# Performance work log

Measured on AMD Instinct MI355X. Metric: run time of the kernel, lower is better.

The kernel has to match this reference:

```python
import jax, jax.numpy as jnp
import numpy as np

H = 2048       # hidden_size
I = 5504       # intermediate_size
E = 8          # num_experts
TOPK = 2       # num_experts_per_tok


def setup_inputs() -> dict:
    key = jax.random.key(0)
    ks = jax.random.split(key, 5)
    s = 0.02
    x = jax.random.normal(ks[0], (2, 2048, H), dtype=jnp.float32)
    router_w = jax.random.normal(ks[1], (E, H), dtype=jnp.float32) * s   # Linear weight [out,in]
    Wg = jax.random.normal(ks[2], (E, I, H), dtype=jnp.float32) * s      # gate_proj per expert
    Wu = jax.random.normal(ks[3], (E, I, H), dtype=jnp.float32) * s      # up_proj per expert
    Wd = jax.random.normal(ks[4], (E, H, I), dtype=jnp.float32) * s      # down_proj per expert
    return {"x": x, "router_w": router_w, "Wg": Wg, "Wu": Wu, "Wd": Wd}


def reference(x, router_w, Wg, Wu, Wd):
    B, S, Hh = x.shape
    xf = x.reshape(-1, Hh)                                  # [T, H]
    logits = xf @ router_w.T                                # [T, E]
    top_vals, top_idx = jax.lax.top_k(logits, TOPK)         # [T, K]
    top_w = jax.nn.softmax(top_vals, axis=-1)               # softmax over selected logits only
    # combine weight per (token, expert): zero if expert not selected
    combine = jnp.sum(jax.nn.one_hot(top_idx, E, dtype=xf.dtype) * top_w[..., None], axis=1)  # [T, E]

    out = jnp.zeros_like(xf)
    for e in range(E):  # fixed small expert loop (unrolled under jit)
        h = jax.nn.silu(xf @ Wg[e].T) * (xf @ Wu[e].T)      # [T, I]
        y = h @ Wd[e].T                                     # [T, H]
        out = out + combine[:, e:e + 1] * y
    return out.reshape(B, S, Hh)
```

## Files before the change

kernel.cpp:

```cpp
#include <hip/hip_runtime.h>
#include <cstdint>
#include <cstddef>

#define HDIM 2048
#define IDIM 5504
#define NEXP 8
#define NTOK 4096
#define NROWS (2 * NTOK)

#define NCT1 86
#define NRT1 10
#define NWG1 (NCT1 * NRT1 * NEXP)
#define NK1  (HDIM / 32)
#define NCT2 8
#define NRT2 10
#define NWG2 (NCT2 * NRT2 * NEXP)
#define NK2  (IDIM / 32)
#define WDCH (NEXP * HDIM * IDIM / 8)

typedef _Float16 half8 __attribute__((ext_vector_type(8)));
typedef _Float16 half4v __attribute__((ext_vector_type(4)));
typedef float floatx4 __attribute__((ext_vector_type(4)));

#define GLOAD16(g, l)                                                         \
  __builtin_amdgcn_global_load_lds(                                           \
      (const __attribute__((address_space(1))) void*)(g),                     \
      (__attribute__((address_space(3))) void*)(l), 16, 0, 0)

#define XH_OFF   0
#define HB_OFF   (XH_OFF + (size_t)NTOK * HDIM * 2)
#define BTOK_OFF (HB_OFF + (size_t)NROWS * IDIM * 2)
#define BW_OFF   (BTOK_OFF + 32768)
#define TOKP_OFF (BW_OFF + 32768)
#define TOKW_OFF (TOKP_OFF + 16384)
#define T2R_OFF  (TOKW_OFF + 32768)
#define META_OFF (T2R_OFF + 32768)
#define Y2_OFF   (META_OFF + 128)
#define WD16_OFF (Y2_OFF + (size_t)NROWS * HDIM * 2)


__global__ void router_kernel(const float* __restrict__ x, const float* __restrict__ rw,
                              _Float16* __restrict__ xh,
                              int* __restrict__ tokp, float2* __restrict__ tokw,
                              int* __restrict__ cnt) {
  int t = blockIdx.x * 4 + (threadIdx.x >> 6);
  int lane = threadIdx.x & 63;
  const float4* xr = (const float4*)(x + (size_t)t * HDIM);
  _Float16* xhr = xh + (size_t)t * HDIM;
  float acc[NEXP];
#pragma unroll
  for (int e = 0; e < NEXP; ++e) acc[e] = 0.f;
#pragma unroll
  for (int it = 0; it < HDIM / 256; ++it) {
    float4 xv = xr[lane + 64 * it];
    half4v hv = { (_Float16)xv.x, (_Float16)xv.y, (_Float16)xv.z, (_Float16)xv.w };
    *(half4v*)(xhr + (lane + 64 * it) * 4) = hv;
#pragma unroll
    for (int e = 0; e < NEXP; ++e) {
      float4 wv = ((const float4*)(rw + (size_t)e * HDIM))[lane + 64 * it];
      acc[e] += xv.x * wv.x + xv.y * wv.y + xv.z * wv.z + xv.w * wv.w;
    }
  }
#pragma unroll
  for (int off = 32; off > 0; off >>= 1) {
#pragma unroll
    for (int e = 0; e < NEXP; ++e) acc[e] += __shfl_xor(acc[e], off);
  }
  if (lane == 0) {
    int e0 = 0; float v0 = acc[0];
#pragma unroll
    for (int e = 1; e < NEXP; ++e) {
      if (acc[e] > v0) { v0 = acc[e]; e0 = e; }
    }
    int e1 = -1; float v1 = -3.0e38f;
#pragma unroll
    for (int e = 0; e < NEXP; ++e) {
      if (e == e0) continue;
      if (acc[e] > v1) { v1 = acc[e]; e1 = e; }
    }
    float w0 = 1.f / (1.f + __expf(v1 - v0));
    tokp[t] = e0 | (e1 << 8);
    tokw[t] = make_float2(w0, 1.f - w0);
    atomicAdd(&cnt[e0], 1);
    atomicAdd(&cnt[e1], 1);
  }
}

__global__ void scan_kernel(const int* __restrict__ cnt, int* __restrict__ offp) {
  if (threadIdx.x == 0) {
    int s = 0;
    for (int e = 0; e < NEXP; ++e) { offp[e] = s; s += cnt[e]; }
    offp[NEXP] = s;
  }
}

__global__ void scatter_kernel(const int* __restrict__ tokp, const float2* __restrict__ tokw,
                               const int* __restrict__ offp, int* __restrict__ cursor,
                               int* __restrict__ btok, float* __restrict__ bw,
                               int* __restrict__ t2r) {
  int t = blockIdx.x * blockDim.x + threadIdx.x;
  if (t >= NTOK) return;
  int p = tokp[t];
  float2 w = tokw[t];
  int e0 = p & 0xff, e1 = (p >> 8) & 0xff;
  int r0 = offp[e0] + atomicAdd(&cursor[e0], 1);
  btok[r0] = t; bw[r0] = w.x; t2r[2 * t] = r0;
  int r1 = offp[e1] + atomicAdd(&cursor[e1], 1);
  btok[r1] = t; bw[r1] = w.y; t2r[2 * t + 1] = r1;
}

__global__ void combine_kernel(const _Float16* __restrict__ y2, const int* __restrict__ t2r,
                               const float2* __restrict__ tokw, float* __restrict__ out) {
  int idx = blockIdx.x * 256 + threadIdx.x;
  int t = idx >> 9, c = (idx & 511) * 4;
  int r0 = t2r[2 * t], r1 = t2r[2 * t + 1];
  float2 w = tokw[t];
  half4v v0 = *(const half4v*)(y2 + (size_t)r0 * HDIM + c);
  half4v v1 = *(const half4v*)(y2 + (size_t)r1 * HDIM + c);
  float4 o;
  o.x = w.x * (float)v0[0] + w.y * (float)v1[0];
  o.y = w.x * (float)v0[1] + w.y * (float)v1[1];
  o.z = w.x * (float)v0[2] + w.y * (float)v1[2];
  o.w = w.x * (float)v0[3] + w.y * (float)v1[3];
  *(float4*)(out + (size_t)t * HDIM + c) = o;
}

__global__ __launch_bounds__(256, 3) void stage1_kernel(
    const _Float16* __restrict__ xh, const float* __restrict__ Wg, const float* __restrict__ Wu,
    const int* __restrict__ offp, const int* __restrict__ btok, _Float16* __restrict__ hb,
    const float* __restrict__ Wd, _Float16* __restrict__ wd16) {
  int bid = blockIdx.x;
  int wg = (bid & 7) * (NWG1 / 8) + (bid >> 3);
  int rt = wg % NRT1;
  int ct = (wg / NRT1) % NCT1;
  int e  = wg / (NRT1 * NCT1);
  int base = offp[e];
  int ne = offp[e + 1] - base;
  int tid = threadIdx.x, lane = tid & 63, wave = tid >> 6;

  if (rt * 128 < ne) {
    int valid = ne - rt * 128; if (valid > 128) valid = 128;

    __shared__ __attribute__((aligned(16))) _Float16 As[2][128 * 32];
    __shared__ __attribute__((aligned(16))) _Float16 Bs[2][128 * 32];

    const char* abase = (const char*)xh;
    uint32_t aoffB[2];
    const float* bsrc[2];
    int bdstB[2];
    size_t eoff = (size_t)e * IDIM * HDIM;
#pragma unroll
    for (int i = 0; i < 2; ++i) {
      int L = wave * 128 + i * 64 + lane;
      int u = L >> 3, sc = (L & 7) ^ (u & 7);
      int r = 2 * u + (sc >> 2), q = sc & 3;
      int rr = (r < valid) ? r : (valid - 1);
      aoffB[i] = (uint32_t)(((uint32_t)btok[base + rt * 128 + rr] * HDIM + q * 8) * 2);
      const float* rp = (r < 64) ? (Wg + eoff + (size_t)(ct * 64 + r) * HDIM)
                                 : (Wu + eoff + (size_t)(ct * 64 + (r - 64)) * HDIM);
      bsrc[i] = rp + q * 8;
      bdstB[i] = L * 16;
    }
    int adst0 = __builtin_amdgcn_readfirstlane(wave * 2048);

    int wm = wave >> 1, wn = wave & 1;
    int lrow = lane & 15, kg = lane >> 4;

    int aoff[4], boff[4];
#pragma unroll
    for (int mi = 0; mi < 4; ++mi) {
      int r = wm * 64 + mi * 16 + lrow;
      int u = r >> 1, cc = (r & 1) * 4 + kg;
      aoff[mi] = u * 64 + ((cc ^ (u & 7)) * 8);
    }
#pragma unroll
    for (int f = 0; f < 4; ++f) {
      int rb = (f < 2) ? (wn * 32 + f * 16 + lrow) : (64 + wn * 32 + (f - 2) * 16 + lrow);
      int u = rb >> 1, cc = (rb & 1) * 4 + kg;
      boff[f] = u * 64 + ((cc ^ (u & 7)) * 8);
    }

    floatx4 acc[4][4] = {};
    floatx4 bp[2][2];

    auto bload = [&](int t) {
#pragma unroll
      for (int i = 0; i < 2; ++i) {
        bp[i][0] = *(const floatx4*)(bsrc[i] + t * 32);
        bp[i][1] = *(const floatx4*)(bsrc[i] + t * 32 + 4);
      }
    };
    auto astage = [&](int t, int buf) {
      uint32_t kb = (uint32_t)t * 64u;
#pragma unroll
      for (int i = 0; i < 2; ++i)
        GLOAD16(abase + (aoffB[i] + kb), (char*)As[buf] + adst0 + i * 1024);
    };
    auto bwrite = [&](int buf) {
#pragma unroll
      for (int i = 0; i < 2; ++i) {
        half8 h = { (_Float16)bp[i][0].x, (_Float16)bp[i][0].y, (_Float16)bp[i][0].z, (_Float16)bp[i][0].w,
                    (_Float16)bp[i][1].x, (_Float16)bp[i][1].y, (_Float16)bp[i][1].z, (_Float16)bp[i][1].w };
        *(half8*)((char*)Bs[buf] + bdstB[i]) = h;
      }
    };
    auto compute = [&](int buf) {
      half8 af[4], bf[4];
#pragma unroll
      for (int mi = 0; mi < 4; ++mi) af[mi] = *(const half8*)&As[buf][aoff[mi]];
#pragma unroll
      for (int f = 0; f < 4; ++f) bf[f] = *(const half8*)&Bs[buf][boff[f]];
#pragma unroll
      for (int mi = 0; mi < 4; ++mi)
#pragma unroll
        for (int f = 0; f < 4; ++f)
          acc[mi][f] = __builtin_amdgcn_mfma_f32_16x16x32_f16(af[mi], bf[f], acc[mi][f], 0, 0, 0);
    };

    int cur = 0;
    bload(0);
    astage(0, 0);
    bwrite(0);
    __syncthreads();
#pragma unroll 2
    for (int t = 0; t < NK1 - 1; ++t) {
      bload(t + 1);
      astage(t + 1, cur ^ 1);
      compute(cur);
      bwrite(cur ^ 1);
      __syncthreads();
      cur ^= 1;
    }
    compute(cur);

    size_t hrow_base = (size_t)(base + rt * 128);
#pragma unroll
    for (int mi = 0; mi < 4; ++mi) {
#pragma unroll
      for (int j = 0; j < 4; ++j) {
        int r = wm * 64 + mi * 16 + kg * 4 + j;
        if (r < valid) {
#pragma unroll
          for (int f = 0; f < 2; ++f) {
            float g = acc[mi][f][j], u = acc[mi][f + 2][j];
            float hv = g / (1.f + __expf(-g)) * u;
            int c = ct * 64 + wn * 32 + f * 16 + lrow;
            hb[(hrow_base + r) * IDIM + c] = (_Float16)hv;
          }
        }
      }
    }
  }

  const float4* wsrc = (const float4*)Wd;
  half8* wdst = (half8*)wd16;
  for (int i = bid * 256 + tid; i < WDCH; i += NWG1 * 256) {
    float4 a = wsrc[2 * i], b = wsrc[2 * i + 1];
    wdst[i] = half8{ (_Float16)a.x, (_Float16)a.y, (_Float16)a.z, (_Float16)a.w,
                     (_Float16)b.x, (_Float16)b.y, (_Float16)b.z, (_Float16)b.w };
  }
}

__global__ __launch_bounds__(512, 4) void stage2_kernel(
    const _Float16* __restrict__ hb, const _Float16* __restrict__ Wd16,
    const int* __restrict__ offp, _Float16* __restrict__ y2) {
  int bid = blockIdx.x;
  int wg = (bid & 7) * (NWG2 / 8) + (bid >> 3);
  int rt = wg % NRT2;
  int ct = (wg / NRT2) % NCT2;
  int e  = wg / (NRT2 * NCT2);
  int base = offp[e];
  int ne = offp[e + 1] - base;
  if (rt * 128 >= ne) return;
  int valid = ne - rt * 128; if (valid > 128) valid = 128;
  int tid = threadIdx.x, lane = tid & 63, wave = tid >> 6;

  __shared__ __attribute__((aligned(16))) _Float16 As[2][128 * 32];
  __shared__ __attribute__((aligned(16))) _Float16 Bs[2][256 * 32];

  const char* abase = (const char*)hb;
  const char* bbase = (const char*)(Wd16 + (size_t)e * HDIM * IDIM);

  uint32_t aoffB, boffB[2];
  {
    int L = tid;
    int u = L >> 3, sc = (L & 7) ^ (u & 7);
    int r = 2 * u + (sc >> 2), q = sc & 3;
    int rr = (r < valid) ? r : (valid - 1);
    aoffB = (uint32_t)(((size_t)(base + rt * 128 + rr) * IDIM + (size_t)q * 8) * 2);
  }
#pragma unroll
  for (int i = 0; i < 2; ++i) {
    int L = i * 512 + tid;
    int u = L >> 3, sc = (L & 7) ^ (u & 7);
    int r = 2 * u + (sc >> 2), q = sc & 3;
    boffB[i] = (uint32_t)(((size_t)(ct * 256 + r) * IDIM + (size_t)q * 8) * 2);
  }
  int adst0 = __builtin_amdgcn_readfirstlane(wave * 1024);

  int wm = wave >> 2, wn = wave & 3;
  int lrow = lane & 15, kg = lane >> 4;

  int aoff[4], boff[4];
#pragma unroll
  for (int mi = 0; mi < 4; ++mi) {
    int r = wm * 64 + mi * 16 + lrow;
    int u = r >> 1, cc = (r & 1) * 4 + kg;
    aoff[mi] = u * 64 + ((cc ^ (u & 7)) * 8);
  }
#pragma unroll
  for (int f = 0; f < 4; ++f) {
    int rb = wn * 64 + f * 16 + lrow;
    int u = rb >> 1, cc = (rb & 1) * 4 + kg;
    boff[f] = u * 64 + ((cc ^ (u & 7)) * 8);
  }

  floatx4 acc[4][4] = {};

  auto stage = [&](int t, int buf) {
    uint32_t kb = (uint32_t)t * 64u;
    GLOAD16(abase + (aoffB + kb), (char*)As[buf] + adst0);
#pragma unroll
    for (int i = 0; i < 2; ++i)
      GLOAD16(bbase + (boffB[i] + kb), (char*)Bs[buf] + i * 8192 + adst0);
  };
  auto compute = [&](int buf) {
    half8 af[4], bf[4];
#pragma unroll
    for (int mi = 0; mi < 4; ++mi) af[mi] = *(const half8*)&As[buf][aoff[mi]];
#pragma unroll
    for (int f = 0; f < 4; ++f) bf[f] = *(const half8*)&Bs[buf][boff[f]];
#pragma unroll
    for (int mi = 0; mi < 4; ++mi)
#pragma unroll
      for (int f = 0; f < 4; ++f)
        acc[mi][f] = __builtin_amdgcn_mfma_f32_16x16x32_f16(af[mi], bf[f], acc[mi][f], 0, 0, 0);
  };

  int cur = 0;
  stage(0, 0);
  __syncthreads();
#pragma unroll 2
  for (int t = 0; t < NK2 - 1; ++t) {
    stage(t + 1, cur ^ 1);
    compute(cur);
    __syncthreads();
    cur ^= 1;
  }
  compute(cur);

#pragma unroll
  for (int mi = 0; mi < 4; ++mi) {
#pragma unroll
    for (int j = 0; j < 4; ++j) {
      int r = wm * 64 + mi * 16 + kg * 4 + j;
      if (r < valid) {
        int grow = base + rt * 128 + r;
#pragma unroll
        for (int f = 0; f < 4; ++f) {
          int c = ct * 256 + wn * 64 + f * 16 + lrow;
          y2[(size_t)grow * HDIM + c] = (_Float16)acc[mi][f][j];
        }
      }
    }
  }
}

extern "C" void kernel_launch(void* const* d_in, const int* in_sizes, int n_in,
                              void* d_out, int out_size, void* d_ws, size_t ws_size,
                              hipStream_t stream) {
  const float* x  = (const float*)d_in[0];
  const float* rw = (const float*)d_in[1];
  const float* Wg = (const float*)d_in[2];
  const float* Wu = (const float*)d_in[3];
  const float* Wd = (const float*)d_in[4];
  float* out = (float*)d_out;

  char* ws = (char*)d_ws;
  _Float16* xh  = (_Float16*)(ws + XH_OFF);
  _Float16* hb  = (_Float16*)(ws + HB_OFF);
  int*      btok = (int*)(ws + BTOK_OFF);
  float*    bwv  = (float*)(ws + BW_OFF);
  int*      tokp = (int*)(ws + TOKP_OFF);
  float2*   tokw = (float2*)(ws + TOKW_OFF);
  int*      t2r  = (int*)(ws + T2R_OFF);
  int*      meta = (int*)(ws + META_OFF);
  _Float16* y2   = (_Float16*)(ws + Y2_OFF);
  _Float16* wd16 = (_Float16*)(ws + WD16_OFF);
  int* cnt = meta;
  int* offp = meta + 8;
  int* cursor = meta + 20;

  hipMemsetAsync(meta, 0, 128, stream);

  router_kernel<<<NTOK / 4, 256, 0, stream>>>(x, rw, xh, tokp, tokw, cnt);
  scan_kernel<<<1, 64, 0, stream>>>(cnt, offp);
  scatter_kernel<<<NTOK / 256, 256, 0, stream>>>(tokp, tokw, offp, cursor, btok, bwv, t2r);

  stage1_kernel<<<NWG1, 256, 0, stream>>>(xh, Wg, Wu, offp, btok, hb, Wd, wd16);
  stage2_kernel<<<NWG2, 512, 0, stream>>>(hb, wd16, offp, y2);
  combine_kernel<<<NTOK * HDIM / 4 / 256, 256, 0, stream>>>(y2, t2r, tokw, out);
}
```

Baseline: 1.188 ms.

## Widen stage1 tile to 128 intermediate columns and split Wd conversion into its own kernel

Stage1 now uses 512-thread blocks, each computing a 128-token by 128-column gate/up tile, which halves the number of column tiles. Each activation tile loaded from global memory is now reused across twice as many weight columns. The fp32-to-fp16 conversion of Wd, which used to be appended to the end of every stage1 block, moves into a separate grid-stride kernel launched before stage1. In exchange there is an extra launch, larger shared memory per block, and a changed occupancy profile under the new launch bounds.

```diff
diff --git a/kernel.cpp b/kernel.cpp
--- a/kernel.cpp
+++ b/kernel.cpp
@@ -8,7 +8,7 @@
 #define NTOK 4096
 #define NROWS (2 * NTOK)
 
-#define NCT1 86
+#define NCT1 43
 #define NRT1 10
 #define NWG1 (NCT1 * NRT1 * NEXP)
 #define NK1  (HDIM / 32)
@@ -16,7 +16,6 @@
 #define NRT2 10
 #define NWG2 (NCT2 * NRT2 * NEXP)
 #define NK2  (IDIM / 32)
-#define WDCH (NEXP * HDIM * IDIM / 8)
 
 typedef _Float16 half8 __attribute__((ext_vector_type(8)));
 typedef _Float16 half4v __attribute__((ext_vector_type(4)));
@@ -38,6 +37,16 @@
 #define Y2_OFF   (META_OFF + 128)
 #define WD16_OFF (Y2_OFF + (size_t)NROWS * HDIM * 2)
 
+
+__global__ void cvt_w_kernel(const float4* __restrict__ w, half8* __restrict__ o, int n8) {
+  int i = blockIdx.x * blockDim.x + threadIdx.x;
+  int st = gridDim.x * blockDim.x;
+  for (; i < n8; i += st) {
+    float4 a = w[2 * i], b = w[2 * i + 1];
+    o[i] = half8{ (_Float16)a.x, (_Float16)a.y, (_Float16)a.z, (_Float16)a.w,
+                  (_Float16)b.x, (_Float16)b.y, (_Float16)b.z, (_Float16)b.w };
+  }
+}
 
 __global__ void router_kernel(const float* __restrict__ x, const float* __restrict__ rw,
                               _Float16* __restrict__ xh,
@@ -125,10 +134,9 @@
   *(float4*)(out + (size_t)t * HDIM + c) = o;
 }
 
-__global__ __launch_bounds__(256, 3) void stage1_kernel(
+__global__ __launch_bounds__(512, 4) void stage1_kernel(
     const _Float16* __restrict__ xh, const float* __restrict__ Wg, const float* __restrict__ Wu,
-    const int* __restrict__ offp, const int* __restrict__ btok, _Float16* __restrict__ hb,
-    const float* __restrict__ Wd, _Float16* __restrict__ wd16) {
+    const int* __restrict__ offp, const int* __restrict__ btok, _Float16* __restrict__ hb) {
   int bid = blockIdx.x;
   int wg = (bid & 7) * (NWG1 / 8) + (bid >> 3);
   int rt = wg % NRT1;
@@ -136,128 +144,121 @@
   int e  = wg / (NRT1 * NCT1);
   int base = offp[e];
   int ne = offp[e + 1] - base;
+  if (rt * 128 >= ne) return;
+  int valid = ne - rt * 128; if (valid > 128) valid = 128;
   int tid = threadIdx.x, lane = tid & 63, wave = tid >> 6;
 
-  if (rt * 128 < ne) {
-    int valid = ne - rt * 128; if (valid > 128) valid = 128;
-
-    __shared__ __attribute__((aligned(16))) _Float16 As[2][128 * 32];
-    __shared__ __attribute__((aligned(16))) _Float16 Bs[2][128 * 32];
-
-    const char* abase = (const char*)xh;
-    uint32_t aoffB[2];
-    const float* bsrc[2];
-    int bdstB[2];
-    size_t eoff = (size_t)e * IDIM * HDIM;
+  __shared__ __attribute__((aligned(16))) _Float16 As[2][128 * 32];
+  __shared__ __attribute__((aligned(16))) _Float16 Bs[2][256 * 32];
+
+  const char* abase = (const char*)xh;
+  uint32_t aoffB;
+  {
+    int L = tid;
+    int u = L >> 3, sc = (L & 7) ^ (u & 7);
+    int r = 2 * u + (sc >> 2), q = sc & 3;
+    int rr = (r < valid) ? r : (valid - 1);
+    aoffB = (uint32_t)(((uint32_t)btok[base + rt * 128 + rr] * HDIM + q * 8) * 2);
+  }
+  const float* bsrc[2];
+  int bdstB[2];
+  size_t eoff = (size_t)e * IDIM * HDIM;
+#pragma unroll
+  for (int i = 0; i < 2; ++i) {
+    int L = i * 512 + tid;
+    int u = L >> 3, sc = (L & 7) ^ (u & 7);
+    int r = 2 * u + (sc >> 2), q = sc & 3;
+    const float* rp = (r < 128) ? (Wg + eoff + (size_t)(ct * 128 + r) * HDIM)
+                                : (Wu + eoff + (size_t)(ct * 128 + (r - 128)) * HDIM);
+    bsrc[i] = rp + q * 8;
+    bdstB[i] = L * 16;
+  }
+  int adst0 = __builtin_amdgcn_readfirstlane(wave * 1024);
+
+  int wm = wave >> 2, wn = wave & 3;
+  int lrow = lane & 15, kg = lane >> 4;
+
+  int aoff[4], boff[4];
+#pragma unroll
+  for (int mi = 0; mi < 4; ++mi) {
+    int r = wm * 64 + mi * 16 + lrow;
+    int u = r >> 1, cc = (r & 1) * 4 + kg;
+    aoff[mi] = u * 64 + ((cc ^ (u & 7)) * 8);
+  }
+#pragma unroll
+  for (int f = 0; f < 4; ++f) {
+    int rb = (f < 2) ? (wn * 32 + f * 16 + lrow) : (128 + wn * 32 + (f - 2) * 16 + lrow);
+    int u = rb >> 1, cc = (rb & 1) * 4 + kg;
+    boff[f] = u * 64 + ((cc ^ (u & 7)) * 8);
+  }
+
+  floatx4 acc[4][4] = {};
+  floatx4 bp[2][2];
+
+  auto bload = [&](int t) {
 #pragma unroll
     for (int i = 0; i < 2; ++i) {
-      int L = wave * 128 + i * 64 + lane;
-      int u = L >> 3, sc = (L & 7) ^ (u & 7);
-      int r = 2 * u + (sc >> 2), q = sc & 3;
-      int rr = (r < valid) ? r : (valid - 1);
-      aoffB[i] = (uint32_t)(((uint32_t)btok[base + rt * 128 + rr] * HDIM + q * 8) * 2);
-      const float* rp = (r < 64) ? (Wg + eoff + (size_t)(ct * 64 + r) * HDIM)
-                                 : (Wu + eoff + (size_t)(ct * 64 + (r - 64)) * HDIM);
-      bsrc[i] = rp + q * 8;
-      bdstB[i] = L * 16;
-    }
-    int adst0 = __builtin_amdgcn_readfirstlane(wave * 2048);
-
-    int wm = wave >> 1, wn = wave & 1;
-    int lrow = lane & 15, kg = lane >> 4;
-
-    int aoff[4], boff[4];
-#pragma unroll
-    for (int mi = 0; mi < 4; ++mi) {
-      int r = wm * 64 + mi * 16 + lrow;
-      int u = r >> 1, cc = (r & 1) * 4 + kg;
-      aoff[mi] = u * 64 + ((cc ^ (u & 7)) * 8);
-    }
-#pragma unroll
-    for (int f = 0; f < 4; ++f) {
-      int rb = (f < 2) ? (wn * 32 + f * 16 + lrow) : (64 + wn * 32 + (f - 2) * 16 + lrow);
-      int u = rb >> 1, cc = (rb & 1) * 4 + kg;
-      boff[f] = u * 64 + ((cc ^ (u & 7)) * 8);
-    }
-
-    floatx4 acc[4][4] = {};
-    floatx4 bp[2][2];
-
-    auto bload = [&](int t) {
-#pragma unroll
-      for (int i = 0; i < 2; ++i) {
-        bp[i][0] = *(const floatx4*)(bsrc[i] + t * 32);
-        bp[i][1] = *(const floatx4*)(bsrc[i] + t * 32 + 4);
-      }
-    };
-    auto astage = [&](int t, int buf) {
-      uint32_t kb = (uint32_t)t * 64u;
-#pragma unroll
-      for (int i = 0; i < 2; ++i)
-        GLOAD16(abase + (aoffB[i] + kb), (char*)As[buf] + adst0 + i * 1024);
-    };
-    auto bwrite = [&](int buf) {
-#pragma unroll
-      for (int i = 0; i < 2; ++i) {
-        half8 h = { (_Float16)bp[i][0].x, (_Float16)bp[i][0].y, (_Float16)bp[i][0].z, (_Float16)bp[i][0].w,
-                    (_Float16)bp[i][1].x, (_Float16)bp[i][1].y, (_Float16)bp[i][1].z, (_Float16)bp[i][1].w };
-        *(half8*)((char*)Bs[buf] + bdstB[i]) = h;
-      }
-    };
-    auto compute = [&](int buf) {
-      half8 af[4], bf[4];
-#pragma unroll
-      for (int mi = 0; mi < 4; ++mi) af[mi] = *(const half8*)&As[buf][aoff[mi]];
-#pragma unroll
-      for (int f = 0; f < 4; ++f) bf[f] = *(const half8*)&Bs[buf][boff[f]];
-#pragma unroll
-      for (int mi = 0; mi < 4; ++mi)
-#pragma unroll
-        for (int f = 0; f < 4; ++f)
-          acc[mi][f] = __builtin_amdgcn_mfma_f32_16x16x32_f16(af[mi], bf[f], acc[mi][f], 0, 0, 0);
-    };
-
-    int cur = 0;
-    bload(0);
-    astage(0, 0);
-    bwrite(0);
+      bp[i][0] = *(const floatx4*)(bsrc[i] + t * 32);
+      bp[i][1] = *(const floatx4*)(bsrc[i] + t * 32 + 4);
+    }
+  };
+  auto astage = [&](int t, int buf) {
+    uint32_t kb = (uint32_t)t * 64u;
+    GLOAD16(abase + (aoffB + kb), (char*)As[buf] + adst0);
+  };
+  auto bwrite = [&](int buf) {
+#pragma unroll
+    for (int i = 0; i < 2; ++i) {
+      half8 h = { (_Float16)bp[i][0].x, (_Float16)bp[i][0].y, (_Float16)bp[i][0].z, (_Float16)bp[i][0].w,
+                  (_Float16)bp[i][1].x, (_Float16)bp[i][1].y, (_Float16)bp[i][1].z, (_Float16)bp[i][1].w };
+      *(half8*)((char*)Bs[buf] + bdstB[i]) = h;
+    }
+  };
+  auto compute = [&](int buf) {
+    half8 af[4], bf[4];
+#pragma unroll
+    for (int mi = 0; mi < 4; ++mi) af[mi] = *(const half8*)&As[buf][aoff[mi]];
+#pragma unroll
+    for (int f = 0; f < 4; ++f) bf[f] = *(const half8*)&Bs[buf][boff[f]];
+#pragma unroll
+    for (int mi = 0; mi < 4; ++mi)
+#pragma unroll
+      for (int f = 0; f < 4; ++f)
+        acc[mi][f] = __builtin_amdgcn_mfma_f32_16x16x32_f16(af[mi], bf[f], acc[mi][f], 0, 0, 0);
+  };
+
+  int cur = 0;
+  bload(0);
+  astage(0, 0);
+  bwrite(0);
+  __syncthreads();
+#pragma unroll 2
+  for (int t = 0; t < NK1 - 1; ++t) {
+    bload(t + 1);
+    astage(t + 1, cur ^ 1);
+    compute(cur);
+    bwrite(cur ^ 1);
     __syncthreads();
-#pragma unroll 2
-    for (int t = 0; t < NK1 - 1; ++t) {
-      bload(t + 1);
-      astage(t + 1, cur ^ 1);
-      compute(cur);
-      bwrite(cur ^ 1);
-      __syncthreads();
-      cur ^= 1;
-    }
-    compute(cur);
-
-    size_t hrow_base = (size_t)(base + rt * 128);
-#pragma unroll
-    for (int mi = 0; mi < 4; ++mi) {
-#pragma unroll
-      for (int j = 0; j < 4; ++j) {
-        int r = wm * 64 + mi * 16 + kg * 4 + j;
-        if (r < valid) {
-#pragma unroll
-          for (int f = 0; f < 2; ++f) {
-            float g = acc[mi][f][j], u = acc[mi][f + 2][j];
-            float hv = g / (1.f + __expf(-g)) * u;
-            int c = ct * 64 + wn * 32 + f * 16 + lrow;
-            hb[(hrow_base + r) * IDIM + c] = (_Float16)hv;
-          }
+    cur ^= 1;
+  }
+  compute(cur);
+
+  size_t hrow_base = (size_t)(base + rt * 128);
+#pragma unroll
+  for (int mi = 0; mi < 4; ++mi) {
+#pragma unroll
+    for (int j = 0; j < 4; ++j) {
+      int r = wm * 64 + mi * 16 + kg * 4 + j;
+      if (r < valid) {
+#pragma unroll
+        for (int f = 0; f < 2; ++f) {
+          float g = acc[mi][f][j], u = acc[mi][f + 2][j];
+          float hv = g / (1.f + __expf(-g)) * u;
+          int c = ct * 128 + wn * 32 + f * 16 + lrow;
+          hb[(hrow_base + r) * IDIM + c] = (_Float16)hv;
         }
       }
     }
-  }
-
-  const float4* wsrc = (const float4*)Wd;
-  half8* wdst = (half8*)wd16;
-  for (int i = bid * 256 + tid; i < WDCH; i += NWG1 * 256) {
-    float4 a = wsrc[2 * i], b = wsrc[2 * i + 1];
-    wdst[i] = half8{ (_Float16)a.x, (_Float16)a.y, (_Float16)a.z, (_Float16)a.w,
-                     (_Float16)b.x, (_Float16)b.y, (_Float16)b.z, (_Float16)b.w };
   }
 }
 
@@ -396,8 +397,10 @@
   router_kernel<<<NTOK / 4, 256, 0, stream>>>(x, rw, xh, tokp, tokw, cnt);
   scan_kernel<<<1, 64, 0, stream>>>(cnt, offp);
   scatter_kernel<<<NTOK / 256, 256, 0, stream>>>(tokp, tokw, offp, cursor, btok, bwv, t2r);
-
-  stage1_kernel<<<NWG1, 256, 0, stream>>>(xh, Wg, Wu, offp, btok, hb, Wd, wd16);
+  cvt_w_kernel<<<2048, 256, 0, stream>>>((const float4*)Wd, (half8*)wd16,
+                                         NEXP * HDIM * IDIM / 8);
+
+  stage1_kernel<<<NWG1, 512, 0, stream>>>(xh, Wg, Wu, offp, btok, hb);
   stage2_kernel<<<NWG2, 512, 0, stream>>>(hb, wd16, offp, y2);
   combine_kernel<<<NTOK * HDIM / 4 / 256, 256, 0, stream>>>(y2, t2r, tokw, out);
 }
```

After: 1.224 ms. +3.0%, slower.
